# Optimization experiments

Hardware: AMD Instinct MI355X
Metric: run time of the kernel (lower is better)

## Reference

```python
import jax, jax.numpy as jnp
import numpy as np

D_MODEL = 1024
N_HEADS = 16
HEAD_DIM = D_MODEL // N_HEADS
D_FF = 4 * D_MODEL
B, T = 2, 2048
EPS = 1e-5


def setup_inputs() -> dict:
    key = jax.random.key(0)
    ks = jax.random.split(key, 12)
    s = 0.02
    x = jax.random.normal(ks[0], (B, T, D_MODEL), dtype=jnp.float32)
    # causal mask: True where attention is disallowed (masked_fill semantics)
    mask = jnp.triu(jnp.ones((T, T), dtype=bool), k=1)[None, None]
    def lin(k, out_d, in_d):
        return jax.random.normal(k, (out_d, in_d), dtype=jnp.float32) * s
    return {
        "x": x,
        "mask": mask,
        "wq_w": lin(ks[1], D_MODEL, D_MODEL), "wq_b": jnp.zeros((D_MODEL,), jnp.float32),
        "wk_w": lin(ks[2], D_MODEL, D_MODEL), "wk_b": jnp.zeros((D_MODEL,), jnp.float32),
        "wv_w": lin(ks[3], D_MODEL, D_MODEL), "wv_b": jnp.zeros((D_MODEL,), jnp.float32),
        "wo_w": lin(ks[4], D_MODEL, D_MODEL), "wo_b": jnp.zeros((D_MODEL,), jnp.float32),
        "fc1_w": lin(ks[5], D_FF, D_MODEL), "fc1_b": jnp.zeros((D_FF,), jnp.float32),
        "fc2_w": lin(ks[6], D_MODEL, D_FF), "fc2_b": jnp.zeros((D_MODEL,), jnp.float32),
        "ln1_g": jnp.ones((D_MODEL,), jnp.float32), "ln1_b": jnp.zeros((D_MODEL,), jnp.float32),
        "ln2_g": jnp.ones((D_MODEL,), jnp.float32), "ln2_b": jnp.zeros((D_MODEL,), jnp.float32),
    }


def _layer_norm(x, g, b):
    mu = jnp.mean(x, axis=-1, keepdims=True)
    var = jnp.mean(jnp.square(x - mu), axis=-1, keepdims=True)
    return (x - mu) * jax.lax.rsqrt(var + EPS) * g + b


def reference(x, mask, wq_w, wq_b, wk_w, wk_b, wv_w, wv_b, wo_w, wo_b,
              fc1_w, fc1_b, fc2_w, fc2_b, ln1_g, ln1_b, ln2_g, ln2_b):
    Bx, Tx, C = x.shape
    # --- attention sub-block (pre-norm) ---
    h = _layer_norm(x, ln1_g, ln1_b)
    q = h @ wq_w.T + wq_b
    k = h @ wk_w.T + wk_b
    v = h @ wv_w.T + wv_b
    # split heads: [B,T,C] -> [B,H,T,Dh]
    def split(t):
        return t.reshape(Bx, Tx, N_HEADS, HEAD_DIM).transpose(0, 2, 1, 3)
    q, k, v = split(q), split(k), split(v)
    scores = jnp.einsum('bhqd,bhkd->bhqk', q, k) / jnp.sqrt(jnp.float32(HEAD_DIM))
    scores = jnp.where(mask, jnp.float32(-1e9), scores)
    attn = jax.nn.softmax(scores, axis=-1)
    ctx = jnp.einsum('bhqk,bhkd->bhqd', attn, v)
    ctx = ctx.transpose(0, 2, 1, 3).reshape(Bx, Tx, C)
    x = x + (ctx @ wo_w.T + wo_b)
    # --- FFN sub-block (pre-norm) ---
    h = _layer_norm(x, ln2_g, ln2_b)
    h = jax.nn.gelu(h @ fc1_w.T + fc1_b, approximate=False)
    x = x + (h @ fc2_w.T + fc2_b)
    return x
```

## Files before the change

kernel.cpp:

```cpp
#include <hip/hip_runtime.h>
#include <stdint.h>

typedef unsigned short u16;
typedef __bf16 bf16x8 __attribute__((ext_vector_type(8)));
typedef float floatx4 __attribute__((ext_vector_type(4)));

#define AS1(p) ((__attribute__((address_space(1))) void*)(void*)(p))
#define AS3(p) ((__attribute__((address_space(3))) void*)(p))

__device__ __forceinline__ u16 f2bf(float f) {
    unsigned u;
    __builtin_memcpy(&u, &f, 4);
    u += 0x7FFF + ((u >> 16) & 1);
    return (u16)(u >> 16);
}
__device__ __forceinline__ u16 f2bf_trunc(float f) {
    unsigned u;
    __builtin_memcpy(&u, &f, 4);
    return (u16)(u >> 16);
}
__device__ __forceinline__ float exp2_fast(float x) {
    return __builtin_amdgcn_exp2f(x);
}
__device__ __forceinline__ float gelu_f(float x) {
    return 0.5f * x * (1.0f + erff(x * 0.70710678118654752f));
}

__global__ __launch_bounds__(256) void conv_w_kernel(
    const float* __restrict__ wq, const float* __restrict__ wk,
    const float* __restrict__ wv, const float* __restrict__ wo,
    const float* __restrict__ f1, const float* __restrict__ f2,
    const float* __restrict__ bq, const float* __restrict__ bk,
    const float* __restrict__ bv, float* __restrict__ qkvb,
    u16* __restrict__ W) {
    const size_t i4 = ((size_t)blockIdx.x * 256 + threadIdx.x) * 4;
    const size_t M1 = 1048576;
    const float* src;
    size_t off;
    if (i4 < M1)            { src = wq; off = i4; }
    else if (i4 < 2 * M1)   { src = wk; off = i4 - M1; }
    else if (i4 < 3 * M1)   { src = wv; off = i4 - 2 * M1; }
    else if (i4 < 4 * M1)   { src = wo; off = i4 - 3 * M1; }
    else if (i4 < 8 * M1)   { src = f1; off = i4 - 4 * M1; }
    else                    { src = f2; off = i4 - 8 * M1; }
    float4 d = *(const float4*)(src + off);
    ushort4 o;
    o.x = f2bf(d.x); o.y = f2bf(d.y); o.z = f2bf(d.z); o.w = f2bf(d.w);
    *(ushort4*)(W + i4) = o;
    if (blockIdx.x == 0) {
        for (int i = threadIdx.x; i < 1024; i += 256) {
            qkvb[i] = bq[i];
            qkvb[1024 + i] = bk[i];
            qkvb[2048 + i] = bv[i];
        }
    }
}

__global__ __launch_bounds__(64) void ln_kernel(const float* __restrict__ X,
                                                const float* __restrict__ G,
                                                const float* __restrict__ Bt,
                                                u16* __restrict__ Y) {
    const int row = blockIdx.x;
    const int lane = threadIdx.x;
    const float* xr = X + (size_t)row * 1024;
    float v[16];
    float s = 0.f;
#pragma unroll
    for (int i = 0; i < 16; ++i) { v[i] = xr[lane + i * 64]; s += v[i]; }
#pragma unroll
    for (int off = 1; off < 64; off <<= 1) s += __shfl_xor(s, off, 64);
    const float mu = s * (1.0f / 1024.0f);
    float ss = 0.f;
#pragma unroll
    for (int i = 0; i < 16; ++i) { float d = v[i] - mu; ss += d * d; }
#pragma unroll
    for (int off = 1; off < 64; off <<= 1) ss += __shfl_xor(ss, off, 64);
    const float rstd = rsqrtf(ss * (1.0f / 1024.0f) + 1e-5f);
    u16* yr = Y + (size_t)row * 1024;
#pragma unroll
    for (int i = 0; i < 16; ++i) {
        int c = lane + i * 64;
        yr[c] = f2bf((v[i] - mu) * rstd * G[c] + Bt[c]);
    }
}

__global__ __launch_bounds__(256, 3) void gemm128_kernel(
    const u16* __restrict__ A, const u16* __restrict__ Bt,
    const float* __restrict__ bias, const float* __restrict__ resid,
    float* __restrict__ C, int M, int N, int K) {
    __shared__ __align__(16) u16 lA[2 * 128 * 64];
    __shared__ __align__(16) u16 lB[2 * 64 * 64];
    const int tid = threadIdx.x;
    const int wave = tid >> 6, lane = tid & 63;
    const int wm = (wave >> 1) * 64;
    const int wn = (wave & 1) * 32;
    const int lr = lane & 15, lk8 = (lane >> 4) * 8;
    const int r0 = (lane >> 4) * 4;
    const int m0 = blockIdx.x * 128, n0 = blockIdx.y * 64;
    const int NT = K >> 6;
    const u16* const Ab = A + (size_t)m0 * K;
    const u16* const Bb = Bt + (size_t)n0 * K;

    const int srow = tid >> 3;
    const int scol = 8 * ((tid & 7) ^ (srow & 7));
    const int sdst = tid * 8;
    const int swz = (lr & 7) << 3;
    const int c0 = lk8 ^ swz;
    const int c1 = (32 + lk8) ^ swz;

    floatx4 acc[4][2];
#pragma unroll
    for (int i = 0; i < 4; ++i)
#pragma unroll
        for (int j = 0; j < 2; ++j) acc[i][j] = floatx4{0.f, 0.f, 0.f, 0.f};
    bf16x8 aF[4][2], bF[2][2];

#define STAGE128(Pb, Tt)                                                       \
    {                                                                          \
        _Pragma("unroll")                                                      \
        for (int l = 0; l < 4; ++l) {                                          \
            const u16* srcA = Ab + (size_t)(l * 32 + srow) * K +               \
                              (size_t)(Tt) * 64 + scol;                        \
            __builtin_amdgcn_global_load_lds(                                  \
                AS1(srcA), AS3(lA + (Pb) * 8192 + l * 2048 + sdst), 16, 0, 0); \
        }                                                                      \
        _Pragma("unroll")                                                      \
        for (int l = 0; l < 2; ++l) {                                          \
            const u16* srcB = Bb + (size_t)(l * 32 + srow) * K +               \
                              (size_t)(Tt) * 64 + scol;                        \
            __builtin_amdgcn_global_load_lds(                                  \
                AS1(srcB), AS3(lB + (Pb) * 4096 + l * 2048 + sdst), 16, 0, 0); \
        }                                                                      \
    }
#define GROUP128(P, T)                                                         \
    {                                                                          \
        if ((T) + 1 < NT) {                                                    \
            STAGE128((P) ^ 1, (T) + 1);                                        \
            asm volatile("s_waitcnt vmcnt(6)" ::: "memory");                   \
        } else {                                                               \
            asm volatile("s_waitcnt vmcnt(0)" ::: "memory");                   \
        }                                                                      \
        asm volatile("s_barrier" ::: "memory");                                \
        _Pragma("unroll")                                                      \
        for (int i = 0; i < 4; ++i) {                                          \
            aF[i][0] = *(const bf16x8*)&lA[(P) * 8192 + (wm + i * 16 + lr) * 64 + c0]; \
            aF[i][1] = *(const bf16x8*)&lA[(P) * 8192 + (wm + i * 16 + lr) * 64 + c1]; \
        }                                                                      \
        _Pragma("unroll")                                                      \
        for (int j = 0; j < 2; ++j) {                                          \
            bF[j][0] = *(const bf16x8*)&lB[(P) * 4096 + (wn + j * 16 + lr) * 64 + c0]; \
            bF[j][1] = *(const bf16x8*)&lB[(P) * 4096 + (wn + j * 16 + lr) * 64 + c1]; \
        }                                                                      \
        asm volatile("s_waitcnt lgkmcnt(0)" ::: "memory");                     \
        __builtin_amdgcn_sched_barrier(0);                                     \
        __builtin_amdgcn_s_setprio(1);                                         \
        _Pragma("unroll")                                                      \
        for (int i = 0; i < 4; ++i)                                            \
            _Pragma("unroll")                                                  \
            for (int j = 0; j < 2; ++j)                                        \
                _Pragma("unroll")                                              \
                for (int kk = 0; kk < 2; ++kk)                                 \
                    acc[i][j] = __builtin_amdgcn_mfma_f32_16x16x32_bf16(       \
                        aF[i][kk], bF[j][kk], acc[i][j], 0, 0, 0);             \
        __builtin_amdgcn_s_setprio(0);                                         \
        asm volatile("s_barrier" ::: "memory");                                \
    }

    STAGE128(0, 0);
    for (int T = 0; T < NT; T += 2) {
        GROUP128(0, T);
        GROUP128(1, T + 1);
    }
#undef GROUP128
#undef STAGE128

#pragma unroll
    for (int i = 0; i < 4; ++i)
#pragma unroll
        for (int j = 0; j < 2; ++j) {
            const int col = n0 + wn + j * 16 + lr;
            const float bv = bias[col];
#pragma unroll
            for (int r = 0; r < 4; ++r) {
                const int row = m0 + wm + i * 16 + r0 + r;
                C[(size_t)row * N + col] =
                    acc[i][j][r] + bv + resid[(size_t)row * N + col];
            }
        }
}

__global__ __launch_bounds__(512, 2) void gemm256_kernel(
    const u16* __restrict__ A, const u16* __restrict__ Bt,
    const float* __restrict__ bias, u16* __restrict__ C,
    int M, int N, int K, int act) {
    extern __shared__ __align__(16) u16 smem[];
    u16* const lA = smem;
    u16* const lB = smem + 32768;
    const int tid = threadIdx.x;
    const int wave = tid >> 6, lane = tid & 63;
    const int wm = (wave >> 2) * 128;
    const int wn = (wave & 3) * 64;
    const int lr = lane & 15, lk8 = (lane >> 4) * 8;
    const int r0 = (lane >> 4) * 4;

    const int gM = M >> 8;
    int bid = blockIdx.x;
    { const int nwg = gridDim.x;
      const int q = nwg >> 3, r = nwg & 7, xcd = bid & 7, lid = bid >> 3;
      bid = (xcd < r ? xcd * (q + 1) : r * (q + 1) + (xcd - r) * q) + lid; }
    const int m0 = (bid % gM) << 8;
    const int n0 = (bid / gM) << 8;

    const int NT = K >> 6;
    const u16* const Ab = A + (size_t)m0 * K;
    const u16* const Bb = Bt + (size_t)n0 * K;

    const int srow = tid >> 3;
    const int scol = 8 * ((tid & 7) ^ (srow & 7));
    const int sdst = tid * 8;
    const int swz = (lr & 7) << 3;
    const int c0 = lk8 ^ swz;
    const int c1 = (32 + lk8) ^ swz;

    floatx4 acc[8][4];
#pragma unroll
    for (int i = 0; i < 8; ++i)
#pragma unroll
        for (int j = 0; j < 4; ++j) acc[i][j] = floatx4{0.f, 0.f, 0.f, 0.f};
    bf16x8 aF[2][4][2];
    bf16x8 bF[4][2];

#define STAGE_HT(ldsbuf, gbase, h, Tt)                                         \
    {                                                                          \
        _Pragma("unroll")                                                      \
        for (int l = 0; l < 2; ++l) {                                          \
            const u16* src = (gbase) + (size_t)((h) * 128 + l * 64 + srow) * K \
                             + (size_t)(Tt) * 64 + scol;                       \
            __builtin_amdgcn_global_load_lds(                                  \
                AS1(src), AS3((ldsbuf) + (h) * 8192 + l * 4096 + sdst), 16, 0, 0); \
        }                                                                      \
    }
#define PH_BAR() asm volatile("s_barrier" ::: "memory")
#define LGKM0()                                                                \
    do { asm volatile("s_waitcnt lgkmcnt(0)" ::: "memory");                    \
         __builtin_amdgcn_sched_barrier(0); } while (0)
#define MFMA_Q(mq, nq)                                                         \
    __builtin_amdgcn_s_setprio(1);                                             \
    _Pragma("unroll")                                                          \
    for (int i = 0; i < 4; ++i)                                                \
        _Pragma("unroll")                                                      \
        for (int j = 0; j < 2; ++j)                                            \
            _Pragma("unroll")                                                  \
            for (int kk = 0; kk < 2; ++kk)                                     \
                acc[(mq) * 4 + i][(nq) * 2 + j] =                              \
                    __builtin_amdgcn_mfma_f32_16x16x32_bf16(                   \
                        aF[mq][i][kk], bF[(nq) * 2 + j][kk],                   \
                        acc[(mq) * 4 + i][(nq) * 2 + j], 0, 0, 0);             \
    __builtin_amdgcn_s_setprio(0);

#define GROUP(P, T)                                                            \
    {                                                                          \
        u16* const lAp = lA + (P) * 16384;                                     \
        u16* const lBp = lB + (P) * 16384;                                     \
        u16* const lBn = lB + ((P) ^ 1) * 16384;                               \
                                                                  \
        _Pragma("unroll")                                                      \
        for (int i = 0; i < 4; ++i) {                                          \
            aF[0][i][0] = *(const bf16x8*)&lAp[(wm + i * 16 + lr) * 64 + c0];  \
            aF[0][i][1] = *(const bf16x8*)&lAp[(wm + i * 16 + lr) * 64 + c1];  \
        }                                                                      \
        _Pragma("unroll")                                                      \
        for (int nf = 0; nf < 4; ++nf) {                                       \
            bF[nf][0] = *(const bf16x8*)&lBp[(wn + nf * 16 + lr) * 64 + c0];   \
            bF[nf][1] = *(const bf16x8*)&lBp[(wn + nf * 16 + lr) * 64 + c1];   \
        }                                                                      \
        if ((T) + 1 < NT) STAGE_HT(lBn, Bb, 0, (T) + 1);                       \
        PH_BAR(); LGKM0();                                                     \
        MFMA_Q(0, 0);                                                          \
        PH_BAR();                                                              \
                                                                  \
        _Pragma("unroll")                                                      \
        for (int i = 0; i < 4; ++i) {                                          \
            aF[1][i][0] = *(const bf16x8*)&lAp[(wm + 64 + i * 16 + lr) * 64 + c0]; \
            aF[1][i][1] = *(const bf16x8*)&lAp[(wm + 64 + i * 16 + lr) * 64 + c1]; \
        }                                                                      \
        if ((T) + 1 < NT) STAGE_HT(lBn, Bb, 1, (T) + 1);                       \
        PH_BAR(); LGKM0();                                                     \
        MFMA_Q(0, 1);                                                          \
        PH_BAR();                                                              \
             \
        if ((T) + 2 < NT) STAGE_HT(lAp, Ab, 0, (T) + 2);                       \
        MFMA_Q(1, 0);                                                          \
                                                                  \
        if ((T) + 2 < NT) STAGE_HT(lAp, Ab, 1, (T) + 2);                       \
        MFMA_Q(1, 1);                                                          \
        if ((T) + 2 < NT) asm volatile("s_waitcnt vmcnt(4)" ::: "memory");     \
        else              asm volatile("s_waitcnt vmcnt(0)" ::: "memory");     \
        PH_BAR();                                                              \
    }

    STAGE_HT(lA, Ab, 0, 0);
    STAGE_HT(lA, Ab, 1, 0);
    STAGE_HT(lB, Bb, 0, 0);
    STAGE_HT(lB, Bb, 1, 0);
    if (NT > 1) {
        STAGE_HT(lA + 16384, Ab, 0, 1);
        STAGE_HT(lA + 16384, Ab, 1, 1);
    }
    asm volatile("s_waitcnt vmcnt(4)" ::: "memory");
    PH_BAR();

    for (int T = 0; T < NT; T += 2) {
        GROUP(0, T);
        GROUP(1, T + 1);
    }
#undef GROUP
#undef MFMA_Q
#undef LGKM0
#undef PH_BAR
#undef STAGE_HT

#pragma unroll
    for (int mq = 0; mq < 2; ++mq)
#pragma unroll
        for (int i = 0; i < 4; ++i)
#pragma unroll
            for (int nf = 0; nf < 4; ++nf) {
                const int col = n0 + wn + nf * 16 + lr;
                const float bv = bias[col];
                floatx4 v = acc[mq * 4 + i][nf];
#pragma unroll
                for (int r = 0; r < 4; ++r) {
                    const int row = m0 + wm + mq * 64 + i * 16 + r0 + r;
                    float x = v[r] + bv;
                    if (act) x = gelu_f(x);
                    C[(size_t)row * N + col] = f2bf(x);
                }
            }
}

__global__ __launch_bounds__(256) void transp_v(const u16* __restrict__ qkv,
                                                u16* __restrict__ vT) {
    __shared__ u16 lT[64 * 64];
    const int bh = blockIdx.x, tt = blockIdx.y;
    const int b = bh >> 4, h = bh & 15;
    const int t0 = tt * 64;
    const int tid = threadIdx.x;
    const int srow = tid >> 3, scol = (tid & 7) * 8;
#pragma unroll
    for (int rr = 0; rr < 2; ++rr) {
        const int row = srow + rr * 32;
        uint4 d4 = *(const uint4*)(qkv + (size_t)(b * 2048 + t0 + row) * 3072 +
                                   2048 + h * 64 + scol);
        const u16* e = (const u16*)&d4;
#pragma unroll
        for (int t = 0; t < 8; ++t) lT[(scol + t) * 64 + row] = e[t];
    }
    __syncthreads();
#pragma unroll
    for (int rr = 0; rr < 2; ++rr) {
        const int row = srow + rr * 32;
        uint4 d4 = *(const uint4*)&lT[row * 64 + scol];
        *(uint4*)(vT + (size_t)(bh * 64 + row) * 2048 + t0 + scol) = d4;
    }
}

__global__ __launch_bounds__(256) void attn_kernel(const u16* __restrict__ qkv,
                                                   const u16* __restrict__ vT,
                                                   u16* __restrict__ O) {
    __shared__ __align__(16) u16 lK[64 * 64];
    __shared__ __align__(16) u16 lV[64 * 64];
    __shared__ __align__(16) u16 lP[4][16 * 64];
    const int tid = threadIdx.x;
    const int wave = tid >> 6, lane = tid & 63;
    const int lr = lane & 15, khi = lane >> 4, lk8 = khi * 8;
    const int p = blockIdx.x;
    const int bh = blockIdx.y;
    const int b = bh >> 4, hh = bh & 15;
    const int rb = b * 2048;
    const size_t vbase = (size_t)(bh * 64) * 2048;
    const int srow = tid >> 3, scol = (tid & 7) * 8;
    const int r0 = khi * 4;
    const int qa = 31 - p, qb = p;
    const int qa0 = qa * 64, qb0 = qb * 64;
    const float C = 0.125f * 1.44269504088896f;

    bf16x8 aqA0, aqA1, aqB0, aqB1;
    {
        const size_t qoffA = (size_t)(rb + qa0 + wave * 16 + lr) * 3072 + hh * 64;
        aqA0 = *(const bf16x8*)(qkv + qoffA + lk8);
        aqA1 = *(const bf16x8*)(qkv + qoffA + 32 + lk8);
        const size_t qoffB = (size_t)(rb + qb0 + wave * 16 + lr) * 3072 + hh * 64;
        aqB0 = *(const bf16x8*)(qkv + qoffB + lk8);
        aqB1 = *(const bf16x8*)(qkv + qoffB + 32 + lk8);
    }

    floatx4 oA[4], oB[4];
    float lA_[4], lB_[4];
#pragma unroll
    for (int r = 0; r < 4; ++r) {
        oA[r] = floatx4{0.f, 0.f, 0.f, 0.f};
        oB[r] = floatx4{0.f, 0.f, 0.f, 0.f};
        lA_[r] = 0.f; lB_[r] = 0.f;
    }

#define TILE_ROUND(aq0_, aq1_, oo_, ll_, q0_, diag_, k0_)                       \
    {                                                                           \
        float s[4][4];                                                          \
        _Pragma("unroll")                                                       \
        for (int j = 0; j < 4; ++j) {                                           \
            bf16x8 bk0 = *(const bf16x8*)&lK[(j * 16 + lr) * 64 + lk8];         \
            bf16x8 bk1 = *(const bf16x8*)&lK[(j * 16 + lr) * 64 + 32 + lk8];    \
            floatx4 t = floatx4{0.f, 0.f, 0.f, 0.f};                            \
            t = __builtin_amdgcn_mfma_f32_16x16x32_bf16(aq0_, bk0, t, 0, 0, 0); \
            t = __builtin_amdgcn_mfma_f32_16x16x32_bf16(aq1_, bk1, t, 0, 0, 0); \
            _Pragma("unroll")                                                   \
            for (int r = 0; r < 4; ++r) s[j][r] = t[r];                         \
        }                                                                       \
        if (diag_) {                                                            \
            _Pragma("unroll")                                                   \
            for (int j = 0; j < 4; ++j)                                         \
                _Pragma("unroll")                                               \
                for (int r = 0; r < 4; ++r)                                     \
                    if ((k0_) + j * 16 + lr > (q0_) + wave * 16 + r0 + r)       \
                        s[j][r] = -1e30f;                                       \
        }                                                                       \
        _Pragma("unroll")                                                       \
        for (int j = 0; j < 4; ++j)                                             \
            _Pragma("unroll")                                                   \
            for (int r = 0; r < 4; ++r) {                                       \
                float pv = exp2_fast(s[j][r] * C);                              \
                ll_[r] += pv;                                                   \
                lP[wave][(r0 + r) * 64 + j * 16 + lr] = f2bf_trunc(pv);         \
            }                                                                   \
        bf16x8 ap0 = *(const bf16x8*)&lP[wave][lr * 64 + lk8];                  \
        bf16x8 ap1 = *(const bf16x8*)&lP[wave][lr * 64 + 32 + lk8];             \
        _Pragma("unroll")                                                       \
        for (int jd = 0; jd < 4; ++jd) {                                        \
            bf16x8 bv0 = *(const bf16x8*)&lV[(jd * 16 + lr) * 64 + lk8];        \
            bf16x8 bv1 = *(const bf16x8*)&lV[(jd * 16 + lr) * 64 + 32 + lk8];   \
            oo_[jd] = __builtin_amdgcn_mfma_f32_16x16x32_bf16(ap0, bv0, oo_[jd], 0, 0, 0); \
            oo_[jd] = __builtin_amdgcn_mfma_f32_16x16x32_bf16(ap1, bv1, oo_[jd], 0, 0, 0); \
        }                                                                       \
    }

    for (int kt = 0; kt <= qa; ++kt) {
        const int k0 = kt * 64;
#pragma unroll
        for (int rr = 0; rr < 2; ++rr) {
            const int row = srow + rr * 32;
            __builtin_amdgcn_global_load_lds(
                AS1(qkv + (size_t)(rb + k0 + row) * 3072 + 1024 + hh * 64 + scol),
                AS3(lK + row * 64 + scol), 16, 0, 0);
            __builtin_amdgcn_global_load_lds(
                AS1(vT + vbase + (size_t)row * 2048 + k0 + scol),
                AS3(lV + row * 64 + scol), 16, 0, 0);
        }
        __syncthreads();

        TILE_ROUND(aqA0, aqA1, oA, lA_, qa0, kt == qa, k0);
        if (kt <= qb)
            TILE_ROUND(aqB0, aqB1, oB, lB_, qb0, kt == qb, k0);

        __syncthreads();
    }
#undef TILE_ROUND

#pragma unroll
    for (int off = 1; off < 16; off <<= 1)
#pragma unroll
        for (int r = 0; r < 4; ++r) {
            lA_[r] += __shfl_xor(lA_[r], off, 64);
            lB_[r] += __shfl_xor(lB_[r], off, 64);
        }

#pragma unroll
    for (int r = 0; r < 4; ++r) {
        const float invA = 1.0f / lA_[r];
        const float invB = 1.0f / lB_[r];
#pragma unroll
        for (int jd = 0; jd < 4; ++jd) {
            const size_t offA = (size_t)(rb + qa0 + wave * 16 + r0 + r) * 1024 +
                                hh * 64 + jd * 16 + lr;
            O[offA] = f2bf(oA[jd][r] * invA);
            const size_t offB = (size_t)(rb + qb0 + wave * 16 + r0 + r) * 1024 +
                                hh * 64 + jd * 16 + lr;
            O[offB] = f2bf(oB[jd][r] * invB);
        }
    }
}

extern "C" void kernel_launch(void* const* d_in, const int* in_sizes, int n_in,
                              void* d_out, int out_size, void* d_ws, size_t ws_size,
                              hipStream_t stream) {
    const float* x     = (const float*)d_in[0];
    const float* wq_w  = (const float*)d_in[2];
    const float* wq_b  = (const float*)d_in[3];
    const float* wk_w  = (const float*)d_in[4];
    const float* wk_b  = (const float*)d_in[5];
    const float* wv_w  = (const float*)d_in[6];
    const float* wv_b  = (const float*)d_in[7];
    const float* wo_w  = (const float*)d_in[8];
    const float* wo_b  = (const float*)d_in[9];
    const float* fc1_w = (const float*)d_in[10];
    const float* fc1_b = (const float*)d_in[11];
    const float* fc2_w = (const float*)d_in[12];
    const float* fc2_b = (const float*)d_in[13];
    const float* ln1_g = (const float*)d_in[14];
    const float* ln1_b = (const float*)d_in[15];
    const float* ln2_g = (const float*)d_in[16];
    const float* ln2_b = (const float*)d_in[17];
    float* out = (float*)d_out;

    char* ws = (char*)d_ws;
    const size_t M1 = 1048576;
    const size_t MB = 1048576;
    u16* Wc    = (u16*)ws;
    u16* wqc   = Wc;
    u16* woc   = Wc + 3 * M1;
    u16* f1c   = Wc + 4 * M1;
    u16* f2c   = Wc + 8 * M1;
    u16* h     = (u16*)(ws + 24 * MB);
    u16* ctx   = h;
    u16* qkv   = (u16*)(ws + 32 * MB);
    u16* vT    = (u16*)(ws + 56 * MB);
    u16* ffh   = (u16*)(ws + 32 * MB);
    float* x1  = (float*)(ws + 64 * MB);
    float* qkvb = x1;
    u16* h2    = h;

    const dim3 blk(256);

    static bool s_attr_done = false;
    if (!s_attr_done) {
        hipFuncSetAttribute(reinterpret_cast<const void*>(gemm256_kernel),
                            hipFuncAttributeMaxDynamicSharedMemorySize, 131072);
        s_attr_done = true;
    }

    conv_w_kernel<<<12288, 256, 0, stream>>>(wq_w, wk_w, wv_w, wo_w, fc1_w, fc2_w,
                                             wq_b, wk_b, wv_b, qkvb, Wc);
    ln_kernel<<<4096, 64, 0, stream>>>(x, ln1_g, ln1_b, h);
    gemm256_kernel<<<dim3(16 * 12), dim3(512), 131072, stream>>>(
        h, wqc, qkvb, qkv, 4096, 3072, 1024, 0);
    transp_v<<<dim3(32, 32), blk, 0, stream>>>(qkv, vT);
    attn_kernel<<<dim3(16, 32), blk, 0, stream>>>(qkv, vT, ctx);
    gemm128_kernel<<<dim3(32, 16), blk, 0, stream>>>(
        ctx, woc, wo_b, x, x1, 4096, 1024, 1024);
    ln_kernel<<<4096, 64, 0, stream>>>(x1, ln2_g, ln2_b, h2);
    gemm256_kernel<<<dim3(16 * 16), dim3(512), 131072, stream>>>(
        h2, f1c, fc1_b, ffh, 4096, 4096, 1024, 1);
    gemm128_kernel<<<dim3(32, 16), blk, 0, stream>>>(
        ffh, f2c, fc2_b, x1, out, 4096, 1024, 4096);
}
```

Before: 371.3 us.

## Double-buffer K/V tiles in attention with XOR-swizzled LDS and MFMA priority

```diff
diff --git a/kernel.cpp b/kernel.cpp
--- a/kernel.cpp
+++ b/kernel.cpp
@@ -368,8 +368,8 @@
 __global__ __launch_bounds__(256) void attn_kernel(const u16* __restrict__ qkv,
                                                    const u16* __restrict__ vT,
                                                    u16* __restrict__ O) {
-    __shared__ __align__(16) u16 lK[64 * 64];
-    __shared__ __align__(16) u16 lV[64 * 64];
+    __shared__ __align__(16) u16 lK[2][64 * 64];
+    __shared__ __align__(16) u16 lV[2][64 * 64];
     __shared__ __align__(16) u16 lP[4][16 * 64];
     const int tid = threadIdx.x;
     const int wave = tid >> 6, lane = tid & 63;
@@ -379,11 +379,17 @@
     const int b = bh >> 4, hh = bh & 15;
     const int rb = b * 2048;
     const size_t vbase = (size_t)(bh * 64) * 2048;
-    const int srow = tid >> 3, scol = (tid & 7) * 8;
     const int r0 = khi * 4;
     const int qa = 31 - p, qb = p;
     const int qa0 = qa * 64, qb0 = qb * 64;
     const float C = 0.125f * 1.44269504088896f;
+
+    const int srow = tid >> 3;
+    const int scol = 8 * ((tid & 7) ^ (srow & 7));
+    const int sdst = tid * 8;
+    const int swz = (lr & 7) << 3;
+    const int cc0 = lk8 ^ swz;
+    const int cc1 = (32 + lk8) ^ swz;
 
     bf16x8 aqA0, aqA1, aqB0, aqB1;
     {
@@ -404,19 +410,36 @@
         lA_[r] = 0.f; lB_[r] = 0.f;
     }
 
-#define TILE_ROUND(aq0_, aq1_, oo_, ll_, q0_, diag_, k0_)                       \
+#define ASTAGE(Pb, kt_)                                                        \
+    {                                                                          \
+        const int k0_ = (kt_) * 64;                                            \
+        _Pragma("unroll")                                                      \
+        for (int rr = 0; rr < 2; ++rr) {                                       \
+            const int row = srow + rr * 32;                                    \
+            __builtin_amdgcn_global_load_lds(                                  \
+                AS1(qkv + (size_t)(rb + k0_ + row) * 3072 + 1024 + hh * 64 + scol), \
+                AS3(lK[Pb] + rr * 2048 + sdst), 16, 0, 0);                     \
+            __builtin_amdgcn_global_load_lds(                                  \
+                AS1(vT + vbase + (size_t)row * 2048 + k0_ + scol),             \
+                AS3(lV[Pb] + rr * 2048 + sdst), 16, 0, 0);                     \
+        }                                                                      \
+    }
+
+#define TILE_ROUND(Pb, aq0_, aq1_, oo_, ll_, q0_, diag_, k0_)                   \
     {                                                                           \
         float s[4][4];                                                          \
+        __builtin_amdgcn_s_setprio(1);                                          \
         _Pragma("unroll")                                                       \
         for (int j = 0; j < 4; ++j) {                                           \
-            bf16x8 bk0 = *(const bf16x8*)&lK[(j * 16 + lr) * 64 + lk8];         \
-            bf16x8 bk1 = *(const bf16x8*)&lK[(j * 16 + lr) * 64 + 32 + lk8];    \
+            bf16x8 bk0 = *(const bf16x8*)&lK[Pb][(j * 16 + lr) * 64 + cc0];     \
+            bf16x8 bk1 = *(const bf16x8*)&lK[Pb][(j * 16 + lr) * 64 + cc1];     \
             floatx4 t = floatx4{0.f, 0.f, 0.f, 0.f};                            \
             t = __builtin_amdgcn_mfma_f32_16x16x32_bf16(aq0_, bk0, t, 0, 0, 0); \
             t = __builtin_amdgcn_mfma_f32_16x16x32_bf16(aq1_, bk1, t, 0, 0, 0); \
             _Pragma("unroll")                                                   \
             for (int r = 0; r < 4; ++r) s[j][r] = t[r];                         \
         }                                                                       \
+        __builtin_amdgcn_s_setprio(0);                                          \
         if (diag_) {                                                            \
             _Pragma("unroll")                                                   \
             for (int j = 0; j < 4; ++j)                                         \
@@ -431,40 +454,43 @@
             for (int r = 0; r < 4; ++r) {                                       \
                 float pv = exp2_fast(s[j][r] * C);                              \
                 ll_[r] += pv;                                                   \
-                lP[wave][(r0 + r) * 64 + j * 16 + lr] = f2bf_trunc(pv);         \
+                lP[wave][(r0 + r) * 64 +                                        \
+                         ((j * 16 + lr) ^ (((r0 + r) & 7) << 3))] =             \
+                    f2bf_trunc(pv);                                             \
             }                                                                   \
-        bf16x8 ap0 = *(const bf16x8*)&lP[wave][lr * 64 + lk8];                  \
-        bf16x8 ap1 = *(const bf16x8*)&lP[wave][lr * 64 + 32 + lk8];             \
+        bf16x8 ap0 = *(const bf16x8*)&lP[wave][lr * 64 + cc0];                  \
+        bf16x8 ap1 = *(const bf16x8*)&lP[wave][lr * 64 + cc1];                  \
+        __builtin_amdgcn_s_setprio(1);                                          \
         _Pragma("unroll")                                                       \
         for (int jd = 0; jd < 4; ++jd) {                                        \
-            bf16x8 bv0 = *(const bf16x8*)&lV[(jd * 16 + lr) * 64 + lk8];        \
-            bf16x8 bv1 = *(const bf16x8*)&lV[(jd * 16 + lr) * 64 + 32 + lk8];   \
+            bf16x8 bv0 = *(const bf16x8*)&lV[Pb][(jd * 16 + lr) * 64 + cc0];    \
+            bf16x8 bv1 = *(const bf16x8*)&lV[Pb][(jd * 16 + lr) * 64 + cc1];    \
             oo_[jd] = __builtin_amdgcn_mfma_f32_16x16x32_bf16(ap0, bv0, oo_[jd], 0, 0, 0); \
             oo_[jd] = __builtin_amdgcn_mfma_f32_16x16x32_bf16(ap1, bv1, oo_[jd], 0, 0, 0); \
         }                                                                       \
-    }
-
+        __builtin_amdgcn_s_setprio(0);                                          \
+    }
+
+    ASTAGE(0, 0);
     for (int kt = 0; kt <= qa; ++kt) {
+        const int P = kt & 1;
         const int k0 = kt * 64;
-#pragma unroll
-        for (int rr = 0; rr < 2; ++rr) {
-            const int row = srow + rr * 32;
-            __builtin_amdgcn_global_load_lds(
-                AS1(qkv + (size_t)(rb + k0 + row) * 3072 + 1024 + hh * 64 + scol),
-                AS3(lK + row * 64 + scol), 16, 0, 0);
-            __builtin_amdgcn_global_load_lds(
-                AS1(vT + vbase + (size_t)row * 2048 + k0 + scol),
-                AS3(lV + row * 64 + scol), 16, 0, 0);
+        if (kt < qa) {
+            ASTAGE(P ^ 1, kt + 1);
+            asm volatile("s_waitcnt vmcnt(4)" ::: "memory");
+        } else {
+            asm volatile("s_waitcnt vmcnt(0)" ::: "memory");
         }
-        __syncthreads();
-
-        TILE_ROUND(aqA0, aqA1, oA, lA_, qa0, kt == qa, k0);
+        asm volatile("s_barrier" ::: "memory");
+
+        TILE_ROUND(P, aqA0, aqA1, oA, lA_, qa0, kt == qa, k0);
         if (kt <= qb)
-            TILE_ROUND(aqB0, aqB1, oB, lB_, qb0, kt == qb, k0);
-
-        __syncthreads();
+            TILE_ROUND(P, aqB0, aqB1, oB, lB_, qb0, kt == qb, k0);
+
+        asm volatile("s_barrier" ::: "memory");
     }
 #undef TILE_ROUND
+#undef ASTAGE
 
 #pragma unroll
     for (int off = 1; off < 16; off <<= 1)
```

New measurement: 360.6 us. 1.03x faster.
